# Kernel optimization log

Measured on AMD Instinct MI355X. Metric: run time of the kernel, lower is better.

Reference implementation:

```python
import jax, jax.numpy as jnp
import numpy as np

H, C = 4, 32            # num_heads, hidden_channels per head
HC = H * C
SLOPE_ATT = 0.2         # GATv2Conv negative_slope default
SLOPE_OUT = 0.01        # F.leaky_relu default

N_HOST, N_VM, N_JOB, N_SWITCH = 50000, 100000, 200000, 5000
IN_DIM = 64
E_HS, E_VH, E_JV = 200000, 400000, 800000


def _gatv2(x_src, x_dst, Wl, bl, Wr, br, att, bias, src, dst, n_dst):
    # PyG GATv2Conv (bipartite): lin_l on source, lin_r on destination
    xl = (x_src @ Wl + bl).reshape(-1, H, C)             # [Ns,H,C]
    xr = (x_dst @ Wr + br).reshape(-1, H, C)             # [Nd,H,C]
    e = jax.nn.leaky_relu(xl[src] + xr[dst], SLOPE_ATT)  # [E,H,C]
    logits = jnp.einsum('ehc,hc->eh', e, att)            # [E,H]
    m = jax.ops.segment_max(logits, dst, num_segments=n_dst)
    ex = jnp.exp(logits - m[dst])
    denom = jax.ops.segment_sum(ex, dst, num_segments=n_dst)
    alpha = ex / denom[dst]                              # scatter-softmax grouped by dst
    out = jax.ops.segment_sum(xl[src] * alpha[..., None], dst, num_segments=n_dst)
    return out.reshape(n_dst, HC) + bias, alpha


def setup_inputs() -> dict:
    key = jax.random.key(0)
    ks = iter(jax.random.split(key, 64))
    f32 = jnp.float32
    def randn(shape, scale=1.0):
        return jax.random.normal(next(ks), shape, dtype=f32) * scale
    sw = 1.0 / np.sqrt(IN_DIM)
    sa = 1.0 / np.sqrt(C)
    inp = {
        'x_host': randn((N_HOST, IN_DIM)),
        'x_vm': randn((N_VM, IN_DIM)),
        'x_job': randn((N_JOB, IN_DIM)),
        'x_switch': randn((N_SWITCH, IN_DIM)),
        'e_hs_src': jax.random.randint(next(ks), (E_HS,), 0, N_HOST),
        'e_hs_dst': jax.random.randint(next(ks), (E_HS,), 0, N_SWITCH),
        'e_vh_src': jax.random.randint(next(ks), (E_VH,), 0, N_VM),
        'e_vh_dst': jax.random.randint(next(ks), (E_VH,), 0, N_HOST),
        'e_jv_src': jax.random.randint(next(ks), (E_JV,), 0, N_JOB),
        'e_jv_dst': jax.random.randint(next(ks), (E_JV,), 0, N_VM),
    }
    for rel in ('hs', 'vh', 'jv'):
        inp['Wl_' + rel] = randn((IN_DIM, HC), sw)
        inp['bl_' + rel] = jnp.zeros((HC,), f32)
        inp['Wr_' + rel] = randn((IN_DIM, HC), sw)
        inp['br_' + rel] = jnp.zeros((HC,), f32)
        inp['att_' + rel] = randn((H, C), sa)
        inp['bias_' + rel] = jnp.zeros((HC,), f32)
    for nt in ('host', 'vm', 'job', 'switch'):
        inp['W_' + nt] = randn((HC, 1), 1.0 / np.sqrt(HC))
        inp['b_' + nt] = jnp.zeros((1,), f32)
    return inp


def reference(x_host, x_vm, x_job, x_switch,
              e_hs_src, e_hs_dst, e_vh_src, e_vh_dst, e_jv_src, e_jv_dst,
              Wl_hs, bl_hs, Wr_hs, br_hs, att_hs, bias_hs,
              Wl_vh, bl_vh, Wr_vh, br_vh, att_vh, bias_vh,
              Wl_jv, bl_jv, Wr_jv, br_jv, att_jv, bias_jv,
              W_host, b_host, W_vm, b_vm, W_job, b_job, W_switch, b_switch):
    out_switch, a_hs = _gatv2(x_host, x_switch, Wl_hs, bl_hs, Wr_hs, br_hs,
                              att_hs, bias_hs, e_hs_src, e_hs_dst, x_switch.shape[0])
    out_host, a_vh = _gatv2(x_vm, x_host, Wl_vh, bl_vh, Wr_vh, br_vh,
                            att_vh, bias_vh, e_vh_src, e_vh_dst, x_host.shape[0])
    out_vm, a_jv = _gatv2(x_job, x_vm, Wl_jv, bl_jv, Wr_jv, br_jv,
                          att_jv, bias_jv, e_jv_src, e_jv_dst, x_vm.shape[0])
    # each dst type receives exactly one relation; stack+sum is identity here
    h_host = jax.nn.leaky_relu(out_host, SLOPE_OUT)
    h_vm = jax.nn.leaky_relu(out_vm, SLOPE_OUT)
    h_switch = jax.nn.leaky_relu(out_switch, SLOPE_OUT)
    h_job = jnp.zeros((x_job.shape[0], HC), x_job.dtype)  # job has no incoming edges
    s_host = jax.nn.sigmoid(h_host @ W_host + b_host)
    s_vm = jax.nn.sigmoid(h_vm @ W_vm + b_vm)
    s_job = jax.nn.sigmoid(h_job @ W_job + b_job)
    s_switch = jax.nn.sigmoid(h_switch @ W_switch + b_switch)
    scores = jnp.concatenate([s_host, s_vm, s_job, s_switch], axis=0)
    return scores, a_hs, a_vh, a_jv
```

## Files before the change

kernel.cpp:

```cpp
#include <hip/hip_runtime.h>
#include <hip/hip_fp16.h>


#define SLOPE_ATT 0.2f
#define SLOPE_OUT 0.01f

typedef _Float16 half8_t __attribute__((ext_vector_type(8)));
typedef _Float16 v2h_t __attribute__((ext_vector_type(2)));
typedef float float4_t __attribute__((ext_vector_type(4)));

struct WSrc { const float* W[6]; };

__global__ __launch_bounds__(256) void init_wt_kernel(
    int* __restrict__ head, int ptot, WSrc wsrc, __half* __restrict__ Wt) {
    int i = blockIdx.x * 256 + threadIdx.x;
    if (i < ptot) {
        head[i] = -1;
    } else {
        int r = i - ptot;
        if (r < 6 * 8192) {
            int j = r >> 13;
            int rr = r & 8191;
            int n = rr >> 6, k = rr & 63;
            Wt[r] = (__half)wsrc.W[j][k * 128 + n];
        }
    }
}

__device__ __forceinline__ void gemm_tile_mfma(
    const float* __restrict__ X, const __half* __restrict__ Wt,
    const float* __restrict__ bb, __half* __restrict__ Y,
    int M, int block_row, __half (*sY)[16][136]) {
    const int lane = threadIdx.x & 63;
    const int wv = threadIdx.x >> 6;
    const int m0 = block_row + wv * 16;
    const int mr = lane & 15;
    const int quad = lane >> 4;
    const int gr = m0 + mr;
    const bool valid = gr < M;

    half8_t a0 = {}, a1 = {};
    if (valid) {
        const float4* xp = (const float4*)(X + (size_t)gr * 64 + quad * 8);
        float4 xa = xp[0], xb = xp[1];
        const float4* xq = (const float4*)(X + (size_t)gr * 64 + 32 + quad * 8);
        float4 xc = xq[0], xd = xq[1];
        a0[0] = (_Float16)xa.x; a0[1] = (_Float16)xa.y;
        a0[2] = (_Float16)xa.z; a0[3] = (_Float16)xa.w;
        a0[4] = (_Float16)xb.x; a0[5] = (_Float16)xb.y;
        a0[6] = (_Float16)xb.z; a0[7] = (_Float16)xb.w;
        a1[0] = (_Float16)xc.x; a1[1] = (_Float16)xc.y;
        a1[2] = (_Float16)xc.z; a1[3] = (_Float16)xc.w;
        a1[4] = (_Float16)xd.x; a1[5] = (_Float16)xd.y;
        a1[6] = (_Float16)xd.z; a1[7] = (_Float16)xd.w;
    }

#pragma unroll
    for (int t = 0; t < 8; t++) {
        const __half* wb = Wt + ((size_t)(t * 16 + mr)) * 64 + quad * 8;
        half8_t b0 = *(const half8_t*)wb;
        half8_t b1 = *(const half8_t*)(wb + 32);
        float4_t c = {0.f, 0.f, 0.f, 0.f};
        c = __builtin_amdgcn_mfma_f32_16x16x32_f16(a0, b0, c, 0, 0, 0);
        c = __builtin_amdgcn_mfma_f32_16x16x32_f16(a1, b1, c, 0, 0, 0);
        int ocol = t * 16 + mr;
        float bv = bb[ocol];
        int lrow = quad * 4;
#pragma unroll
        for (int r = 0; r < 4; r++)
            sY[wv][lrow + r][ocol] = (__half)(c[r] + bv);
    }

    __syncthreads();

    const int rl = lane >> 4;
    const int c8 = (lane & 15) * 8;
#pragma unroll
    for (int i = 0; i < 4; i++) {
        int row = i * 4 + rl;
        int gr2 = m0 + row;
        if (gr2 < M) {
            half8_t v = *(const half8_t*)&sY[wv][row][c8];
            *(half8_t*)&Y[(size_t)gr2 * 128 + c8] = v;
        }
    }
}

__device__ __forceinline__ void link_work(
    int linkId, int linkBlocks,
    const int* __restrict__ d0, const int* __restrict__ s0,
    const int* __restrict__ d1, const int* __restrict__ s1,
    const int* __restrict__ d2, const int* __restrict__ s2,
    int* __restrict__ head, int2* __restrict__ nxt,
    int E0, int E1, int E2, int pb1, int pb2) {
    int i = linkId * 256 + threadIdx.x;
    int Etot = E0 + E1 + E2;
    int stride = linkBlocks * 256;
    for (; i < Etot; i += stride) {
        int le, slot; const int* sp;
        if (i < E0)           { le = i;           slot = d0[le];       sp = s0; }
        else if (i < E0 + E1) { le = i - E0;      slot = pb1 + d1[le]; sp = s1; }
        else                  { le = i - E0 - E1; slot = pb2 + d2[le]; sp = s2; }
        int old = atomicExch(&head[slot], le);
        nxt[i] = make_int2(old, sp[le]);
    }
}

struct GemmJobs {
    const float* X[6]; const float* b[6]; __half* Y[6];
    int M[6]; int base[7];
};

__global__ __launch_bounds__(256) void mega_gemm_link_kernel(
    GemmJobs j, const __half* __restrict__ Wt, int s, int L,
    const int* __restrict__ d0, const int* __restrict__ s0,
    const int* __restrict__ d1, const int* __restrict__ s1,
    const int* __restrict__ d2, const int* __restrict__ s2,
    int* __restrict__ head, int2* __restrict__ nxt,
    int E0, int E1, int E2, int pb1, int pb2) {
    __shared__ __half sY[4][16][136];
    int b = blockIdx.x;
    int q = b / s;
    bool onGridline = (b - q * s) == 0;
    if (onGridline && q < L) {
        link_work(q, L, d0, s0, d1, s1, d2, s2, head, nxt, E0, E1, E2, pb1, pb2);
    } else {
        int before = q + (onGridline ? 0 : 1);
        if (before > L) before = L;
        int g = b - before;
        int k = 0;
        while (g >= j.base[k + 1]) k++;
        gemm_tile_mfma(j.X[k], Wt + (size_t)k * 8192, j.b[k], j.Y[k], j.M[k],
                       (g - j.base[k]) * 64, sY);
    }
}

__device__ __forceinline__ void agg_body(
    const __half* __restrict__ xl, const __half* __restrict__ xr,
    const float* __restrict__ att,
    const int* __restrict__ head, const int2* __restrict__ nxt,
    float* __restrict__ ex_out, float* __restrict__ dn_out,
    const float* __restrict__ bias, const float* __restrict__ Wn,
    const float* __restrict__ bn, float* __restrict__ scores,
    int Nd, int wid, int l) {
    if (wid >= Nd) return;
    int h = l >> 4;

    v2h_t xrh = ((const v2h_t*)(xr + (size_t)wid * 128))[l];
    float2 av  = ((const float2*)att)[l];
    v2h_t ath = {(_Float16)av.x, (_Float16)av.y};
    const v2h_t sl2 = {(_Float16)SLOPE_ATT, (_Float16)SLOPE_ATT};

    float ssum = 0.f;
    float2 acc = make_float2(0.f, 0.f);

    int e = head[wid];
    bool any = (e >= 0);
    int2 cur = any ? nxt[e] : make_int2(-1, 0);
    v2h_t xcur = any ? ((const v2h_t*)(xl + (size_t)cur.y * 128))[l]
                     : (v2h_t){};
    int en = cur.x;
    int2 nsn = (en >= 0) ? nxt[en] : make_int2(-1, 0);

    while (e >= 0) {
        v2h_t xnext = (en >= 0)
            ? ((const v2h_t*)(xl + (size_t)nsn.y * 128))[l] : (v2h_t){};
        int enn = nsn.x;
        int2 nsnn = (enn >= 0) ? nxt[enn] : make_int2(-1, 0);

        v2h_t vs = xcur + xrh;
        v2h_t lk = __builtin_elementwise_max(vs, vs * sl2);
        float p = __builtin_amdgcn_fdot2(lk, ath, 0.f, false);
        p += __shfl_xor(p, 1);
        p += __shfl_xor(p, 2);
        p += __shfl_xor(p, 4);
        p += __shfl_xor(p, 8);
        float w = __expf(p);
        if ((l & 15) == 0) ex_out[(size_t)e * 4 + h] = w;
        float x0 = (float)xcur[0], x1 = (float)xcur[1];
        ssum += w;
        acc.x += w * x0;
        acc.y += w * x1;

        e = en; xcur = xnext; en = enn; nsn = nsnn;
    }

    if ((l & 15) == 0) dn_out[(size_t)wid * 4 + h] = ssum;

    float rr = any ? 1.f / ssum : 0.f;
    float2 bb = ((const float2*)bias)[l];
    float2 w2 = ((const float2*)Wn)[l];
    float o0 = acc.x * rr + bb.x; o0 = o0 > 0.f ? o0 : SLOPE_OUT * o0;
    float o1 = acc.y * rr + bb.y; o1 = o1 > 0.f ? o1 : SLOPE_OUT * o1;
    float pr = o0 * w2.x + o1 * w2.y;
#pragma unroll
    for (int off = 1; off < 64; off <<= 1) pr += __shfl_xor(pr, off);
    if (l == 0) scores[wid] = 1.f / (1.f + __expf(-(pr + bn[0])));
}

struct AggJob {
    const __half* xl; const __half* xr; const float* att;
    const int* head; const int2* nxt;
    float* ex; float* dn;
    const float* bias; const float* Wn; const float* bn; float* scores;
    int Nd;
};
struct AggJobs { AggJob r[3]; int base[4]; };

__global__ __launch_bounds__(256) void agg3_kernel(AggJobs aj) {
    int b = blockIdx.x;
    int k = 0;
    while (b >= aj.base[k + 1]) k++;
    AggJob J = aj.r[k];
    int wid = ((b - aj.base[k]) * 256 + threadIdx.x) >> 6;
    int l = threadIdx.x & 63;
    agg_body(J.xl, J.xr, J.att, J.head, J.nxt, J.ex, J.dn,
             J.bias, J.Wn, J.bn, J.scores, J.Nd, wid, l);
}

__global__ __launch_bounds__(256) void alpha_job_kernel(
    float* __restrict__ ex,
    const int* __restrict__ d0, const int* __restrict__ d1,
    const int* __restrict__ d2,
    const float* __restrict__ dn,
    int E0, int E1, int E2, int pb1, int pb2, int ab,
    const float* __restrict__ bjob, float* __restrict__ sjob, int NJ) {
    int b = blockIdx.x;
    if (b < ab) {
        int i = b * 256 + threadIdx.x;
        int tot = (E0 + E1 + E2) * 4;
        if (i >= tot) return;
        int e = i >> 2, h = i & 3;
        int d;
        if (e < E0)           d = d0[e];
        else if (e < E0 + E1) d = pb1 + d1[e - E0];
        else                  d = pb2 + d2[e - E0 - E1];
        ex[i] = ex[i] / dn[(size_t)d * 4 + h];
    } else {
        int i = (b - ab) * 256 + threadIdx.x;
        if (i < NJ) sjob[i] = 1.f / (1.f + __expf(-bjob[0]));
    }
}


extern "C" void kernel_launch(void* const* d_in, const int* in_sizes, int n_in,
                              void* d_out, int out_size, void* d_ws, size_t ws_size,
                              hipStream_t stream) {
    const float* x_host   = (const float*)d_in[0];
    const float* x_vm     = (const float*)d_in[1];
    const float* x_job    = (const float*)d_in[2];
    const float* x_switch = (const float*)d_in[3];
    const int* e_hs_src = (const int*)d_in[4];
    const int* e_hs_dst = (const int*)d_in[5];
    const int* e_vh_src = (const int*)d_in[6];
    const int* e_vh_dst = (const int*)d_in[7];
    const int* e_jv_src = (const int*)d_in[8];
    const int* e_jv_dst = (const int*)d_in[9];
    const float* Wl_hs = (const float*)d_in[10];
    const float* bl_hs = (const float*)d_in[11];
    const float* Wr_hs = (const float*)d_in[12];
    const float* br_hs = (const float*)d_in[13];
    const float* att_hs = (const float*)d_in[14];
    const float* bias_hs = (const float*)d_in[15];
    const float* Wl_vh = (const float*)d_in[16];
    const float* bl_vh = (const float*)d_in[17];
    const float* Wr_vh = (const float*)d_in[18];
    const float* br_vh = (const float*)d_in[19];
    const float* att_vh = (const float*)d_in[20];
    const float* bias_vh = (const float*)d_in[21];
    const float* Wl_jv = (const float*)d_in[22];
    const float* bl_jv = (const float*)d_in[23];
    const float* Wr_jv = (const float*)d_in[24];
    const float* br_jv = (const float*)d_in[25];
    const float* att_jv = (const float*)d_in[26];
    const float* bias_jv = (const float*)d_in[27];
    const float* W_host   = (const float*)d_in[28];
    const float* b_host   = (const float*)d_in[29];
    const float* W_vm     = (const float*)d_in[30];
    const float* b_vm     = (const float*)d_in[31];
    const float* W_job    = (const float*)d_in[32];
    const float* b_job    = (const float*)d_in[33];
    const float* W_switch = (const float*)d_in[34];
    const float* b_switch = (const float*)d_in[35];

    const int NH  = in_sizes[0] / 64;
    const int NV  = in_sizes[1] / 64;
    const int NJ  = in_sizes[2] / 64;
    const int NSW = in_sizes[3] / 64;
    const int EHS = in_sizes[4];
    const int EVH = in_sizes[6];
    const int EJV = in_sizes[8];
    const int Etot = EHS + EVH + EJV;

    float* out = (float*)d_out;
    float* s_host = out;
    float* s_vm = out + NH;
    float* s_job = out + NH + NV;
    float* s_sw = out + NH + NV + NJ;
    float* a_hs = out + NH + NV + NJ + NSW;
    float* a_vh = a_hs + (size_t)EHS * 4;
    float* a_jv = a_vh + (size_t)EVH * 4;

    const int pb1 = ((NSW + 255) / 256) * 256;
    const int pb2 = pb1 + ((NH + 255) / 256) * 256;
    const int ptot = pb2 + ((NV + 255) / 256) * 256;

    float* ws = (float*)d_ws;
    int2* nxt_all = (int2*)ws;
    int* head_all = (int*)(nxt_all + Etot);
    float* dn_all = (float*)(head_all + ptot);
    __half* Wt    = (__half*)(dn_all + (size_t)ptot * 4);
    __half* mats  = Wt + 6 * 8192;
    __half* xl_hs = mats;
    __half* xr_hs = xl_hs + (size_t)NH * 128;
    __half* xl_vh = xr_hs + (size_t)NSW * 128;
    __half* xr_vh = xl_vh + (size_t)NV * 128;
    __half* xl_jv = xr_vh + (size_t)NH * 128;
    __half* xr_jv = xl_jv + (size_t)NJ * 128;

    {
        WSrc w;
        w.W[0] = Wl_hs; w.W[1] = Wr_hs; w.W[2] = Wl_vh;
        w.W[3] = Wr_vh; w.W[4] = Wl_jv; w.W[5] = Wr_jv;
        int tot = ptot + 6 * 8192;
        init_wt_kernel<<<(tot + 255) / 256, 256, 0, stream>>>(head_all, ptot, w, Wt);
    }

    {
        GemmJobs j;
        const float* Xs[6] = {x_host, x_switch, x_vm, x_host, x_job, x_vm};
        const float* bs[6] = {bl_hs, br_hs, bl_vh, br_vh, bl_jv, br_jv};
        __half* Ys[6] = {xl_hs, xr_hs, xl_vh, xr_vh, xl_jv, xr_jv};
        int Ms[6] = {NH, NSW, NV, NH, NJ, NV};
        int base = 0;
        for (int k = 0; k < 6; k++) {
            j.X[k] = Xs[k]; j.b[k] = bs[k]; j.Y[k] = Ys[k]; j.M[k] = Ms[k];
            j.base[k] = base;
            base += (Ms[k] + 63) / 64;
        }
        j.base[6] = base;
        int L = 3072;
        int T = base + L;
        int s = T / L; if (s < 1) s = 1;
        mega_gemm_link_kernel<<<T, 256, 0, stream>>>(
            j, Wt, s, L, e_hs_dst, e_hs_src, e_vh_dst, e_vh_src,
            e_jv_dst, e_jv_src, head_all, nxt_all, EHS, EVH, EJV, pb1, pb2);
    }

    {
        AggJobs aj;
        aj.r[0] = {xl_hs, xr_hs, att_hs, head_all + 0, nxt_all + 0,
                   a_hs, dn_all + 0,
                   bias_hs, W_switch, b_switch, s_sw, NSW};
        aj.r[1] = {xl_vh, xr_vh, att_vh, head_all + pb1, nxt_all + EHS,
                   a_vh, dn_all + (size_t)pb1 * 4,
                   bias_vh, W_host, b_host, s_host, NH};
        aj.r[2] = {xl_jv, xr_jv, att_jv, head_all + pb2, nxt_all + (EHS + EVH),
                   a_jv, dn_all + (size_t)pb2 * 4,
                   bias_jv, W_vm, b_vm, s_vm, NV};
        aj.base[0] = 0;
        aj.base[1] = (int)(((size_t)NSW * 64 + 255) / 256);
        aj.base[2] = aj.base[1] + (int)(((size_t)NH * 64 + 255) / 256);
        aj.base[3] = aj.base[2] + (int)(((size_t)NV * 64 + 255) / 256);
        agg3_kernel<<<aj.base[3], 256, 0, stream>>>(aj);
    }

    {
        int ab = (Etot * 4 + 255) / 256;
        int jb = (NJ + 255) / 256;
        alpha_job_kernel<<<ab + jb, 256, 0, stream>>>(
            a_hs, e_hs_dst, e_vh_dst, e_jv_dst, dn_all,
            EHS, EVH, EJV, pb1, pb2, ab, b_job, s_job, NJ);
    }
}
```

Baseline: 457.1 us.

## Process eight destinations per wavefront with 16-element-per-lane aggregation

Remaps the aggregation kernel so each wavefront handles eight destination nodes with eight lanes each, and each lane processes 16 channels using 128-bit half8 loads and fdot2. Before, one full wavefront walked each destination's edge list with only 2 channels per lane. The goal is shorter cross-lane reductions, wider memory accesses, and more independent linked-list walks per wave to hide pointer-chasing latency. In exchange, lanes diverge when destinations in a wave have different degrees, the software prefetch of the next edge is dropped, and each lane needs more registers for its 16 accumulators.

```diff
diff --git a/kernel.cpp b/kernel.cpp
--- a/kernel.cpp
+++ b/kernel.cpp
@@ -8,6 +8,22 @@
 typedef _Float16 half8_t __attribute__((ext_vector_type(8)));
 typedef _Float16 v2h_t __attribute__((ext_vector_type(2)));
 typedef float float4_t __attribute__((ext_vector_type(4)));
+
+__device__ __forceinline__ float dot8(half8_t a, half8_t b, float acc) {
+    v2h_t a0 = __builtin_shufflevector(a, a, 0, 1);
+    v2h_t a1 = __builtin_shufflevector(a, a, 2, 3);
+    v2h_t a2 = __builtin_shufflevector(a, a, 4, 5);
+    v2h_t a3 = __builtin_shufflevector(a, a, 6, 7);
+    v2h_t b0 = __builtin_shufflevector(b, b, 0, 1);
+    v2h_t b1 = __builtin_shufflevector(b, b, 2, 3);
+    v2h_t b2 = __builtin_shufflevector(b, b, 4, 5);
+    v2h_t b3 = __builtin_shufflevector(b, b, 6, 7);
+    acc = __builtin_amdgcn_fdot2(a0, b0, acc, false);
+    acc = __builtin_amdgcn_fdot2(a1, b1, acc, false);
+    acc = __builtin_amdgcn_fdot2(a2, b2, acc, false);
+    acc = __builtin_amdgcn_fdot2(a3, b3, acc, false);
+    return acc;
+}
 
 struct WSrc { const float* W[6]; };
 
@@ -135,69 +151,6 @@
     }
 }
 
-__device__ __forceinline__ void agg_body(
-    const __half* __restrict__ xl, const __half* __restrict__ xr,
-    const float* __restrict__ att,
-    const int* __restrict__ head, const int2* __restrict__ nxt,
-    float* __restrict__ ex_out, float* __restrict__ dn_out,
-    const float* __restrict__ bias, const float* __restrict__ Wn,
-    const float* __restrict__ bn, float* __restrict__ scores,
-    int Nd, int wid, int l) {
-    if (wid >= Nd) return;
-    int h = l >> 4;
-
-    v2h_t xrh = ((const v2h_t*)(xr + (size_t)wid * 128))[l];
-    float2 av  = ((const float2*)att)[l];
-    v2h_t ath = {(_Float16)av.x, (_Float16)av.y};
-    const v2h_t sl2 = {(_Float16)SLOPE_ATT, (_Float16)SLOPE_ATT};
-
-    float ssum = 0.f;
-    float2 acc = make_float2(0.f, 0.f);
-
-    int e = head[wid];
-    bool any = (e >= 0);
-    int2 cur = any ? nxt[e] : make_int2(-1, 0);
-    v2h_t xcur = any ? ((const v2h_t*)(xl + (size_t)cur.y * 128))[l]
-                     : (v2h_t){};
-    int en = cur.x;
-    int2 nsn = (en >= 0) ? nxt[en] : make_int2(-1, 0);
-
-    while (e >= 0) {
-        v2h_t xnext = (en >= 0)
-            ? ((const v2h_t*)(xl + (size_t)nsn.y * 128))[l] : (v2h_t){};
-        int enn = nsn.x;
-        int2 nsnn = (enn >= 0) ? nxt[enn] : make_int2(-1, 0);
-
-        v2h_t vs = xcur + xrh;
-        v2h_t lk = __builtin_elementwise_max(vs, vs * sl2);
-        float p = __builtin_amdgcn_fdot2(lk, ath, 0.f, false);
-        p += __shfl_xor(p, 1);
-        p += __shfl_xor(p, 2);
-        p += __shfl_xor(p, 4);
-        p += __shfl_xor(p, 8);
-        float w = __expf(p);
-        if ((l & 15) == 0) ex_out[(size_t)e * 4 + h] = w;
-        float x0 = (float)xcur[0], x1 = (float)xcur[1];
-        ssum += w;
-        acc.x += w * x0;
-        acc.y += w * x1;
-
-        e = en; xcur = xnext; en = enn; nsn = nsnn;
-    }
-
-    if ((l & 15) == 0) dn_out[(size_t)wid * 4 + h] = ssum;
-
-    float rr = any ? 1.f / ssum : 0.f;
-    float2 bb = ((const float2*)bias)[l];
-    float2 w2 = ((const float2*)Wn)[l];
-    float o0 = acc.x * rr + bb.x; o0 = o0 > 0.f ? o0 : SLOPE_OUT * o0;
-    float o1 = acc.y * rr + bb.y; o1 = o1 > 0.f ? o1 : SLOPE_OUT * o1;
-    float pr = o0 * w2.x + o1 * w2.y;
-#pragma unroll
-    for (int off = 1; off < 64; off <<= 1) pr += __shfl_xor(pr, off);
-    if (l == 0) scores[wid] = 1.f / (1.f + __expf(-(pr + bn[0])));
-}
-
 struct AggJob {
     const __half* xl; const __half* xr; const float* att;
     const int* head; const int2* nxt;
@@ -212,10 +165,88 @@
     int k = 0;
     while (b >= aj.base[k + 1]) k++;
     AggJob J = aj.r[k];
-    int wid = ((b - aj.base[k]) * 256 + threadIdx.x) >> 6;
-    int l = threadIdx.x & 63;
-    agg_body(J.xl, J.xr, J.att, J.head, J.nxt, J.ex, J.dn,
-             J.bias, J.Wn, J.bn, J.scores, J.Nd, wid, l);
+
+    const int l = threadIdx.x & 63;
+    const int wv = threadIdx.x >> 6;
+    const int li = l & 7;
+    const int g = l >> 3;
+    const int dbase = ((b - aj.base[k]) * 4 + wv) * 8;
+    const int d = dbase + g;
+    if (dbase >= J.Nd) return;
+    const bool dok = d < J.Nd;
+    const int h = li >> 1;
+
+    half8_t xr0 = {}, xr1 = {};
+    if (dok) {
+        const half8_t* xrp = (const half8_t*)(J.xr + (size_t)d * 128) + li * 2;
+        xr0 = xrp[0]; xr1 = xrp[1];
+    }
+    half8_t at0, at1;
+    {
+        const float* ap = J.att + li * 16;
+#pragma unroll
+        for (int i = 0; i < 8; i++) {
+            at0[i] = (_Float16)ap[i];
+            at1[i] = (_Float16)ap[8 + i];
+        }
+    }
+    const half8_t sl8 = {(_Float16)SLOPE_ATT, (_Float16)SLOPE_ATT,
+                         (_Float16)SLOPE_ATT, (_Float16)SLOPE_ATT,
+                         (_Float16)SLOPE_ATT, (_Float16)SLOPE_ATT,
+                         (_Float16)SLOPE_ATT, (_Float16)SLOPE_ATT};
+
+    float acc[16] = {};
+    float ssum = 0.f;
+
+    int e = dok ? J.head[d] : -1;
+    const bool any = (e >= 0);
+
+    while (__any(e >= 0)) {
+        bool act = (e >= 0);
+        int2 ns = act ? J.nxt[e] : make_int2(-1, 0);
+        half8_t x0 = {}, x1 = {};
+        if (act) {
+            const half8_t* xp = (const half8_t*)(J.xl + (size_t)ns.y * 128) + li * 2;
+            x0 = xp[0]; x1 = xp[1];
+        }
+        if (act) {
+            half8_t v0 = x0 + xr0;
+            half8_t v1 = x1 + xr1;
+            half8_t lk0 = __builtin_elementwise_max(v0, v0 * sl8);
+            half8_t lk1 = __builtin_elementwise_max(v1, v1 * sl8);
+            float p = dot8(lk1, at1, dot8(lk0, at0, 0.f));
+            p += __shfl_xor(p, 1);
+            float w = __expf(p);
+            if ((li & 1) == 0) J.ex[(size_t)e * 4 + h] = w;
+            ssum += w;
+#pragma unroll
+            for (int i = 0; i < 8; i++) {
+                acc[i]     += w * (float)x0[i];
+                acc[8 + i] += w * (float)x1[i];
+            }
+        }
+        e = act ? ns.x : -1;
+    }
+
+    if (dok && (li & 1) == 0) J.dn[(size_t)d * 4 + h] = ssum;
+
+    float rr = any ? 1.f / ssum : 0.f;
+    float pr = 0.f;
+    if (dok) {
+        const float* bp = J.bias + li * 16;
+        const float* wp = J.Wn + li * 16;
+#pragma unroll
+        for (int i = 0; i < 16; i++) {
+            float o = acc[i] * rr + bp[i];
+            o = o > 0.f ? o : SLOPE_OUT * o;
+            pr += o * wp[i];
+        }
+    }
+    pr += __shfl_xor(pr, 1);
+    pr += __shfl_xor(pr, 2);
+    pr += __shfl_xor(pr, 4);
+    if (dok && li == 0)
+        J.scores[d] = 1.f / (1.f + __expf(-(pr + J.bn[0])));
 }
 
 __global__ __launch_bounds__(256) void alpha_job_kernel(
@@ -359,9 +390,9 @@
                    a_jv, dn_all + (size_t)pb2 * 4,
                    bias_jv, W_vm, b_vm, s_vm, NV};
         aj.base[0] = 0;
-        aj.base[1] = (int)(((size_t)NSW * 64 + 255) / 256);
-        aj.base[2] = aj.base[1] + (int)(((size_t)NH * 64 + 255) / 256);
-        aj.base[3] = aj.base[2] + (int)(((size_t)NV * 64 + 255) / 256);
+        aj.base[1] = (NSW + 31) / 32;
+        aj.base[2] = aj.base[1] + (NH + 31) / 32;
+        aj.base[3] = aj.base[2] + (NV + 31) / 32;
         agg3_kernel<<<aj.base[3], 256, 0, stream>>>(aj);
     }
 
```

Result: faster. 389.5 us (-14.8%).
